# Kernel tuning notes

Measured on AMD Instinct MI355X. Metric: run time of the kernel, lower is better.

## Reference

```python
import jax, jax.numpy as jnp
import numpy as np

B, F, D, K = 16384, 200, 32, 4
H1, H2 = 32, 16
BN_EPS = 1e-3  # keras BatchNormalization default epsilon


def setup_inputs() -> dict:
    key = jax.random.key(0)
    ks = jax.random.split(key, 12)
    inp = {
        "x": jax.random.normal(ks[0], (B, F, D), dtype=jnp.float32),
        "tag_embedding": jax.random.normal(ks[1], (B, D), dtype=jnp.float32),
        "vk_embs": jax.random.normal(ks[2], (D, K), dtype=jnp.float32) * 0.1,
        # tower 1: Dense(D->H1) stacked over K experts, + BN params
        "W1": jax.random.normal(ks[3], (K, D, H1), dtype=jnp.float32) * (1.0 / np.sqrt(D)),
        "b1": jnp.zeros((K, H1), dtype=jnp.float32),
        "g1": jnp.ones((K, H1), dtype=jnp.float32) + 0.1 * jax.random.normal(ks[4], (K, H1), dtype=jnp.float32),
        "be1": 0.1 * jax.random.normal(ks[5], (K, H1), dtype=jnp.float32),
        "m1": 0.1 * jax.random.normal(ks[6], (K, H1), dtype=jnp.float32),
        "v1": jax.random.uniform(ks[7], (K, H1), dtype=jnp.float32, minval=0.5, maxval=1.5),
        # tower 2: Dense(H1->H2) + BN params
        "W2": jax.random.normal(ks[8], (K, H1, H2), dtype=jnp.float32) * (1.0 / np.sqrt(H1)),
        "b2": jnp.zeros((K, H2), dtype=jnp.float32),
        "g2": jnp.ones((K, H2), dtype=jnp.float32) + 0.1 * jax.random.normal(ks[9], (K, H2), dtype=jnp.float32),
        "be2": 0.1 * jax.random.normal(ks[10], (K, H2), dtype=jnp.float32),
        "m2": 0.1 * jax.random.normal(ks[11], (K, H2), dtype=jnp.float32),
        "v2": jnp.ones((K, H2), dtype=jnp.float32),
    }
    return inp


def _bn(h, gamma, beta, mean, var):
    # inference-mode batch norm per expert, broadcast over batch: h [B,K,H]
    return (h - mean) * jax.lax.rsqrt(var + BN_EPS) * gamma + beta


def reference(x, tag_embedding, vk_embs, W1, b1, g1, be1, m1, v1,
              W2, b2, g2, be2, m2, v2):
    scale = 1.0 / jnp.sqrt(jnp.float32(D))
    # attention-pooled per-kernel context (dropout = identity in eval mode)
    vk_scores = jnp.einsum('bfd,dk->bkf', x, vk_embs)          # [B,K,F]
    vk_probs = jax.nn.softmax(vk_scores, axis=-1)
    context = jnp.einsum('bkf,bfd->bkd', vk_probs, x) * scale   # [B,K,D]
    # per-expert MLP towers, batched over K: Dense -> BN -> relu (dropout=id)
    h = jnp.einsum('bkd,kdh->bkh', context, W1) + b1            # [B,K,H1]
    h = jax.nn.relu(_bn(h, g1, be1, m1, v1))
    h = jnp.einsum('bkh,khj->bkj', h, W2) + b2                  # [B,K,H2]
    vk_outs = jax.nn.relu(_bn(h, g2, be2, m2, v2))
    # soft gate from tag embedding
    gate_scores = (tag_embedding @ vk_embs) * scale             # [B,K]
    gate_probs = jax.nn.softmax(gate_scores, axis=-1)[:, :, None]
    user_embedding = jnp.sum(vk_outs * gate_probs, axis=1)      # [B,H2]
    return user_embedding
```

## Files before the change

kernel.cpp:

```cpp
#include <hip/hip_runtime.h>
#include <hip/hip_bf16.h>

#define NF 200
#define ND 32
#define NK 4
#define NH1 32
#define NH2 16
#define BN_EPS 1e-3f

template<int CTRL>
__device__ __forceinline__ float dpp_add(float v) {
  const int r = __builtin_amdgcn_update_dpp(0, __float_as_int(v), CTRL, 0xF, 0xF, true);
  return v + __int_as_float(r);
}

__global__ __launch_bounds__(256, 8) void mvke_fused(
    const float* __restrict__ x, const float* __restrict__ tag,
    const float* __restrict__ vk,
    const float* __restrict__ W1, const float* __restrict__ b1,
    const float* __restrict__ g1, const float* __restrict__ be1,
    const float* __restrict__ m1, const float* __restrict__ v1,
    const float* __restrict__ W2, const float* __restrict__ b2,
    const float* __restrict__ g2, const float* __restrict__ be2,
    const float* __restrict__ m2, const float* __restrict__ v2,
    float* __restrict__ out, int nrows)
{
  __shared__ float ctx_s[4][NK*ND];
  __shared__ float h1_s[4][NK*NH1];

  const int tid  = threadIdx.x;
  const int wave = tid >> 6;
  const int lane = tid & 63;
  const int fg   = lane >> 3;
  const int dl   = lane & 7;
  const int row  = blockIdx.x * 4 + wave;
  const bool live = (row < nrows);

  float vkt[NK][4];
  #pragma unroll
  for (int j = 0; j < 4; ++j) {
    const float4 vv = *(const float4*)(vk + (4*dl + j) * NK);
    vkt[0][j] = vv.x; vkt[1][j] = vv.y; vkt[2][j] = vv.z; vkt[3][j] = vv.w;
  }

  const float* xrow = x + (size_t)(live ? row : 0) * (NF*ND);
  const int laneoff = fg*ND + dl*4;

  float cx[NK], cy[NK], cz[NK], cw[NK], ls[NK];
  #pragma unroll
  for (int k = 0; k < NK; ++k) { cx[k]=cy[k]=cz[k]=cw[k]=ls[k]=0.f; }

  float4 xa = *(const float4*)(xrow + laneoff);
  for (int it = 0; it < NF/8; ++it) {
    float4 xn;
    if (it + 1 < NF/8)
      xn = *(const float4*)(xrow + (it+1)*(8*ND) + laneoff);
    #pragma unroll
    for (int k = 0; k < NK; ++k) {
      float t = xa.x*vkt[k][0] + xa.y*vkt[k][1] + xa.z*vkt[k][2] + xa.w*vkt[k][3];
      t = dpp_add<0xB1>(t);
      t = dpp_add<0x4E>(t);
      t = dpp_add<0x141>(t);
      const float p = __expf(t);
      ls[k] += p;
      cx[k] = fmaf(p, xa.x, cx[k]);
      cy[k] = fmaf(p, xa.y, cy[k]);
      cz[k] = fmaf(p, xa.z, cz[k]);
      cw[k] = fmaf(p, xa.w, cw[k]);
    }
    xa = xn;
  }

  #pragma unroll
  for (int k = 0; k < NK; ++k) {
    ls[k] = dpp_add<0x128>(ls[k]);
    cx[k] = dpp_add<0x128>(cx[k]);
    cy[k] = dpp_add<0x128>(cy[k]);
    cz[k] = dpp_add<0x128>(cz[k]);
    cw[k] = dpp_add<0x128>(cw[k]);
    #pragma unroll
    for (int m = 16; m <= 32; m <<= 1) {
      ls[k] += __shfl_xor(ls[k], m);
      cx[k] += __shfl_xor(cx[k], m);
      cy[k] += __shfl_xor(cy[k], m);
      cz[k] += __shfl_xor(cz[k], m);
      cw[k] += __shfl_xor(cw[k], m);
    }
  }

  const float scale = 0.17677669529663687f;
  if (fg == 0) {
    #pragma unroll
    for (int k = 0; k < NK; ++k) {
      const float inv = scale / ls[k];
      float* p = &ctx_s[wave][k*ND + dl*4];
      p[0] = cx[k]*inv; p[1] = cy[k]*inv; p[2] = cz[k]*inv; p[3] = cw[k]*inv;
    }
  }
  __syncthreads();

  #pragma unroll
  for (int rep = 0; rep < 2; ++rep) {
    const int o = lane + rep*64;
    const int k = o >> 5, h = o & 31;
    const float* wp = W1 + k*(ND*NH1) + h;
    const float* cp = &ctx_s[wave][k*ND];
    float acc = 0.f;
    #pragma unroll
    for (int d = 0; d < ND; ++d) acc = fmaf(cp[d], wp[d*NH1], acc);
    const float a = g1[o] * rsqrtf(v1[o] + BN_EPS);
    const float c = fmaf(b1[o] - m1[o], a, be1[o]);
    h1_s[wave][o] = fmaxf(fmaf(acc, a, c), 0.f);
  }
  __syncthreads();

  {
    const int k3 = lane >> 4, j3 = lane & 15;
    const float* wp = W2 + k3*(NH1*NH2) + j3;
    const float* hp = &h1_s[wave][k3*NH1];
    float acc = 0.f;
    #pragma unroll
    for (int h = 0; h < NH1; ++h) acc = fmaf(hp[h], wp[h*NH2], acc);
    const int o = k3*NH2 + j3;
    const float a2 = g2[o] * rsqrtf(v2[o] + BN_EPS);
    const float c2 = fmaf(b2[o] - m2[o], a2, be2[o]);
    const float h2v = fmaxf(fmaf(acc, a2, c2), 0.f);

    const float* tp = tag + (size_t)(live ? row : 0) * ND;
    float gs0=0.f, gs1=0.f, gs2=0.f, gs3=0.f;
    #pragma unroll
    for (int d = 0; d < ND; ++d) {
      const float t = tp[d];
      const float4 vv = *(const float4*)(vk + d*NK);
      gs0 = fmaf(t, vv.x, gs0);
      gs1 = fmaf(t, vv.y, gs1);
      gs2 = fmaf(t, vv.z, gs2);
      gs3 = fmaf(t, vv.w, gs3);
    }
    gs0 *= scale; gs1 *= scale; gs2 *= scale; gs3 *= scale;
    const float mx = fmaxf(fmaxf(gs0, gs1), fmaxf(gs2, gs3));
    const float e0 = __expf(gs0-mx), e1 = __expf(gs1-mx),
                e2 = __expf(gs2-mx), e3 = __expf(gs3-mx);
    const float esum = e0 + e1 + e2 + e3;
    const float ek = (k3 == 0) ? e0 : (k3 == 1) ? e1 : (k3 == 2) ? e2 : e3;

    float val = (ek / esum) * h2v;
    val += __shfl_xor(val, 16);
    val += __shfl_xor(val, 32);
    if (live && lane < NH2) out[(size_t)row*NH2 + lane] = val;
  }
}

extern "C" void kernel_launch(void* const* d_in, const int* in_sizes, int n_in,
                              void* d_out, int out_size, void* d_ws, size_t ws_size,
                              hipStream_t stream) {
  const float* x   = (const float*)d_in[0];
  const float* tag = (const float*)d_in[1];
  const float* vk  = (const float*)d_in[2];
  const float* W1  = (const float*)d_in[3];
  const float* b1  = (const float*)d_in[4];
  const float* g1  = (const float*)d_in[5];
  const float* be1 = (const float*)d_in[6];
  const float* m1  = (const float*)d_in[7];
  const float* v1  = (const float*)d_in[8];
  const float* W2  = (const float*)d_in[9];
  const float* b2  = (const float*)d_in[10];
  const float* g2  = (const float*)d_in[11];
  const float* be2 = (const float*)d_in[12];
  const float* m2  = (const float*)d_in[13];
  const float* v2  = (const float*)d_in[14];
  float* out = (float*)d_out;

  const int nrows = in_sizes[1] / ND;
  const int nblocks = (nrows + 3) / 4;
  mvke_fused<<<nblocks, 256, 0, stream>>>(x, tag, vk, W1, b1, g1, be1, m1, v1,
                                          W2, b2, g2, be2, m2, v2, out, nrows);
}
```

Measured before the change: 108.0 us.

## Stream x rows into LDS via async global_load_lds with 4-deep ring buffer

Replaces the register double-buffered float4 loads of x with direct global-to-LDS DMA (global_load_lds, 16 bytes per lane) into a 4-stage per-wave ring buffer. Explicit vmcnt waits keep up to four chunks in flight, hiding memory latency behind the exp/FMA work. It adds 16 KB of LDS per block, which may cap occupancy, and the hand-written waitcnt sequencing must stay consistent with other outstanding vector loads.

```diff
diff --git a/kernel.cpp b/kernel.cpp
--- a/kernel.cpp
+++ b/kernel.cpp
@@ -7,12 +7,22 @@
 #define NH1 32
 #define NH2 16
 #define BN_EPS 1e-3f
+#define DEPTH 4
+#define NIT   25
 
 template<int CTRL>
 __device__ __forceinline__ float dpp_add(float v) {
   const int r = __builtin_amdgcn_update_dpp(0, __float_as_int(v), CTRL, 0xF, 0xF, true);
   return v + __int_as_float(r);
 }
+
+__device__ __forceinline__ void dma16(const float* g, float* l) {
+  __builtin_amdgcn_global_load_lds(
+      (const __attribute__((address_space(1))) float*)g,
+      (__attribute__((address_space(3))) float*)l, 16, 0, 0);
+}
+
+#define WAITV(N) asm volatile("s_waitcnt vmcnt(" #N ")" ::: "memory")
 
 __global__ __launch_bounds__(256, 8) void mvke_fused(
     const float* __restrict__ x, const float* __restrict__ tag,
@@ -25,6 +35,7 @@
     const float* __restrict__ m2, const float* __restrict__ v2,
     float* __restrict__ out, int nrows)
 {
+  __shared__ float xbuf[4][DEPTH][256];
   __shared__ float ctx_s[4][NK*ND];
   __shared__ float h1_s[4][NK*NH1];
 
@@ -44,31 +55,40 @@
   }
 
   const float* xrow = x + (size_t)(live ? row : 0) * (NF*ND);
-  const int laneoff = fg*ND + dl*4;
 
   float cx[NK], cy[NK], cz[NK], cw[NK], ls[NK];
   #pragma unroll
   for (int k = 0; k < NK; ++k) { cx[k]=cy[k]=cz[k]=cw[k]=ls[k]=0.f; }
 
-  float4 xa = *(const float4*)(xrow + laneoff);
-  for (int it = 0; it < NF/8; ++it) {
-    float4 xn;
-    if (it + 1 < NF/8)
-      xn = *(const float4*)(xrow + (it+1)*(8*ND) + laneoff);
+  #pragma unroll
+  for (int s = 0; s < DEPTH; ++s)
+    dma16(xrow + s*256 + lane*4, &xbuf[wave][s][0]);
+
+  #pragma unroll
+  for (int t = 0; t < NIT; ++t) {
+    if (t <= NIT-DEPTH)      { WAITV(3); }
+    else if (t == NIT-3)     { WAITV(2); }
+    else if (t == NIT-2)     { WAITV(1); }
+    else                     { WAITV(0); }
+
+    const float4 xa = *(const float4*)&xbuf[wave][t & (DEPTH-1)][lane*4];
+
+    if (t + DEPTH < NIT)
+      dma16(xrow + (t+DEPTH)*256 + lane*4, &xbuf[wave][t & (DEPTH-1)][0]);
+
     #pragma unroll
     for (int k = 0; k < NK; ++k) {
-      float t = xa.x*vkt[k][0] + xa.y*vkt[k][1] + xa.z*vkt[k][2] + xa.w*vkt[k][3];
-      t = dpp_add<0xB1>(t);
-      t = dpp_add<0x4E>(t);
-      t = dpp_add<0x141>(t);
-      const float p = __expf(t);
+      float t0 = xa.x*vkt[k][0] + xa.y*vkt[k][1] + xa.z*vkt[k][2] + xa.w*vkt[k][3];
+      t0 = dpp_add<0xB1>(t0);
+      t0 = dpp_add<0x4E>(t0);
+      t0 = dpp_add<0x141>(t0);
+      const float p = __expf(t0);
       ls[k] += p;
       cx[k] = fmaf(p, xa.x, cx[k]);
       cy[k] = fmaf(p, xa.y, cy[k]);
       cz[k] = fmaf(p, xa.z, cz[k]);
       cw[k] = fmaf(p, xa.w, cw[k]);
     }
-    xa = xn;
   }
 
   #pragma unroll
```

Result: slower. 260.8 us (+141.4%).
